# Kernel optimization log

Measured on AMD Instinct MI355X. Metric: run time of the kernel, lower is better.

## Reference

```python
import jax, jax.numpy as jnp
import numpy as np
from jax import lax

T, B, I, N, C, L = 512, 256, 64, 512, 10, 3
TAU = 2.0  # train_tau=False -> constant, non-trainable


def setup_inputs() -> dict:
    key = jax.random.key(0)
    ks = jax.random.split(key, 12)
    f32 = jnp.float32
    data = jax.random.normal(ks[0], (T, B, I), f32)
    h0 = 0.1 * jax.random.uniform(ks[1], (L, B, N), f32)  # matches 0.1*torch.rand init
    # Linear params; weights stored as [in, out] so y = x @ W + b
    Win = jax.random.normal(ks[2], (I, N), f32) / np.float32(np.sqrt(I))
    b_in = 0.01 * jax.random.normal(ks[3], (N,), f32)
    Whh = jax.random.normal(ks[4], (L, N, N), f32) / np.float32(np.sqrt(N))
    b_hh = 0.01 * jax.random.normal(ks[5], (L, N), f32)
    Whi = jax.random.normal(ks[6], (L - 1, N, N), f32) / np.float32(np.sqrt(N))
    b_hi = 0.01 * jax.random.normal(ks[7], (L - 1, N), f32)
    Wfc = jax.random.normal(ks[8], (N, C), f32) / np.float32(np.sqrt(N))
    b_fc = 0.01 * jax.random.normal(ks[9], (C,), f32)
    return {"data": data, "h0": h0, "Win": Win, "b_in": b_in,
            "Whh": Whh, "b_hh": b_hh, "Whi": Whi, "b_hi": b_hi,
            "Wfc": Wfc, "b_fc": b_fc}


def reference(data, h0, Win, b_in, Whh, b_hh, Whi, b_hi, Wfc, b_fc):
    alpha = 1.0 - 1.0 / TAU
    # forward() zeroes the recurrent diagonal every call
    Whh = Whh * (1.0 - jnp.eye(N, dtype=Whh.dtype))
    x = data @ Win + b_in  # [T, B, N] input projection (single input layer, mean over 1)

    def step(hs, inp):
        h0_, h1_, h2_ = hs
        # layer 0: leaky integration + LeakyReLU; same inp fed to every layer
        n0 = jax.nn.leaky_relu(alpha * h0_ + (h0_ @ Whh[0] + b_hh[0] + inp) / TAU)
        # layer 1 sees the *updated* layer-0 state (sequential within a timestep)
        n1 = jax.nn.leaky_relu(
            alpha * h1_ + (h1_ @ Whh[1] + b_hh[1] + n0 @ Whi[0] + b_hi[0] + inp) / TAU)
        n2 = jax.nn.leaky_relu(
            alpha * h2_ + (h2_ @ Whh[2] + b_hh[2] + n1 @ Whi[1] + b_hi[1] + inp) / TAU)
        return (n0, n1, n2), None

    hs_final, _ = lax.scan(step, (h0[0], h0[1], h0[2]), x)
    out = hs_final[-1] @ Wfc + b_fc  # [B, C], single readout head
    return out
```

## Files before the change

### kernel.cpp

```cpp
#include <hip/hip_runtime.h>
#include <stdint.h>


#define TS    512
#define BB    256
#define NN    512
#define MR    16
#define NRG   16
#define NCT   4
#define RD    8

#define SW(r, c) (((r) << 9) + ((((c) ^ ((r) & 7))) << 3))

typedef __attribute__((ext_vector_type(8))) short s8v;
typedef __attribute__((ext_vector_type(4))) float f4v;
typedef __attribute__((ext_vector_type(4))) unsigned int u4v;

#define MFMA16(a, b, c) __builtin_amdgcn_mfma_f32_16x16x32_bf16((a), (b), (c), 0, 0, 0)

__device__ __forceinline__ short f2bf(float f) {
  union { float f; unsigned u; } v; v.f = f;
  unsigned u = v.u;
  u += 0x7fffu + ((u >> 16) & 1u);
  return (short)(u >> 16);
}

__device__ __forceinline__ s8v pack8(f4v a, f4v b) {
  s8v v;
  v[0] = f2bf(a[0]); v[1] = f2bf(a[1]); v[2] = f2bf(a[2]); v[3] = f2bf(a[3]);
  v[4] = f2bf(b[0]); v[5] = f2bf(b[1]); v[6] = f2bf(b[2]); v[7] = f2bf(b[3]);
  return v;
}

__device__ __forceinline__ void waitvm0() {
  asm volatile("s_waitcnt vmcnt(0)" ::: "memory");
}

__device__ __forceinline__ void stg_sc1_b16(unsigned short* p, unsigned v) {
  asm volatile("global_store_short %0, %1, off sc1" :: "v"(p), "v"(v) : "memory");
}
__device__ __forceinline__ unsigned agent_ld(const unsigned* p) {
  return __hip_atomic_load(p, __ATOMIC_RELAXED, __HIP_MEMORY_SCOPE_AGENT);
}
__device__ __forceinline__ void agent_st(unsigned* p, unsigned v) {
  __hip_atomic_store(p, v, __ATOMIC_RELAXED, __HIP_MEMORY_SCOPE_AGENT);
}

__device__ __forceinline__ void ld4_dual(u4v o[4],
    unsigned vA, unsigned vB,
    const unsigned short* sq, const unsigned short* sp) {
  asm volatile(
      "global_load_dwordx4 %0, %4, %6 sc1\n\t"
      "global_load_dwordx4 %1, %5, %6 sc1\n\t"
      "global_load_dwordx4 %2, %4, %7 sc1\n\t"
      "global_load_dwordx4 %3, %5, %7 sc1\n\t"
      "s_waitcnt vmcnt(0)"
      : "=&v"(o[0]), "=&v"(o[1]), "=&v"(o[2]), "=&v"(o[3])
      : "v"(vA), "v"(vB), "s"(sq), "s"(sp)
      : "memory");
}
__device__ __forceinline__ void ld2_sync(u4v o[2],
    unsigned vA, unsigned vB, const unsigned short* sb) {
  asm volatile(
      "global_load_dwordx4 %0, %2, %4 sc1\n\t"
      "global_load_dwordx4 %1, %3, %4 sc1\n\t"
      "s_waitcnt vmcnt(0)"
      : "=&v"(o[0]), "=&v"(o[1])
      : "v"(vA), "v"(vB), "s"(sb)
      : "memory");
}

__global__ __launch_bounds__(512, 2) void rnn_pipe(
    const float* __restrict__ data, const float* __restrict__ h0,
    const float* __restrict__ Win,  const float* __restrict__ b_in,
    const float* __restrict__ Whh,  const float* __restrict__ b_hh,
    const float* __restrict__ Whi,  const float* __restrict__ b_hi,
    unsigned short* __restrict__ ring, unsigned* __restrict__ cnt,
    float* __restrict__ hfinal)
{
  __shared__ __attribute__((aligned(16))) unsigned short qtile[MR * NN];
  __shared__ __attribute__((aligned(16))) unsigned short ptile[MR * NN];

  const int bi   = blockIdx.x;
  const int x8   = bi & 7;
  const int rr   = bi >> 3;
  const int half = (rr >= 12) ? 1 : 0;
  const int m    = rr - half * 12;
  const int rg   = x8 * 2 + half;
  const int lay  = m >> 2;
  const int ct   = m & 3;
  const int tid  = threadIdx.x;
  const int wv   = tid >> 6;
  const int lane = tid & 63;
  const int lo   = lane & 15;
  const int q4   = lane >> 4;
  const int row0 = rg * MR;
  const int cw   = ct * 128 + wv * 16;

  const int sidx = (lay * NRG + rg) * NCT + ct;
  unsigned* selfprod = cnt + (size_t)sidx * 32;
  unsigned* selfdone = cnt + (size_t)(256 + sidx) * 32;

  unsigned* pollptr = selfprod;
  int polltype = 0;
  if (lane < 4) {
    pollptr = cnt + (size_t)((lay * NRG + rg) * NCT + lane) * 32;  polltype = 1;
  } else if (lane >= 4 && lane < 8 && lay > 0) {
    pollptr = cnt + (size_t)(((lay - 1) * NRG + rg) * NCT + (lane - 4)) * 32;  polltype = 2;
  } else if (lane >= 8 && lane < 12 && lay < 2) {
    pollptr = cnt + (size_t)(256 + ((lay + 1) * NRG + rg) * NCT + (lane - 8)) * 32;  polltype = 3;
  }

  s8v WH[16];
  s8v WI[16];
  s8v WX[2];
  float biasv;
  f4v  hst;

  {
    const float* WmH = Whh + (size_t)lay * NN * NN;
    const int col = cw + lo;
    #pragma unroll
    for (int kk = 0; kk < 16; ++kk) {
      s8v v;
      #pragma unroll
      for (int j = 0; j < 8; ++j) {
        const int k = kk * 32 + q4 * 8 + j;
        float f = WmH[(size_t)k * NN + col];
        if (k == col) f = 0.f;
        v[j] = f2bf(f);
      }
      WH[kk] = v;
    }
    if (lay > 0) {
      const float* WmI = Whi + (size_t)(lay - 1) * NN * NN;
      #pragma unroll
      for (int kk = 0; kk < 16; ++kk) {
        s8v v;
        #pragma unroll
        for (int j = 0; j < 8; ++j)
          v[j] = f2bf(WmI[(size_t)(kk * 32 + q4 * 8 + j) * NN + col]);
        WI[kk] = v;
      }
    }
    #pragma unroll
    for (int kk = 0; kk < 2; ++kk) {
      s8v v;
      #pragma unroll
      for (int j = 0; j < 8; ++j)
        v[j] = f2bf(Win[(size_t)(kk * 32 + q4 * 8 + j) * NN + col]);
      WX[kk] = v;
    }
    float b = b_hh[lay * NN + col] + b_in[col];
    if (lay > 0) b += b_hi[(lay - 1) * NN + col];
    biasv = b;
    #pragma unroll
    for (int r = 0; r < 4; ++r)
      hst[r] = h0[(size_t)lay * BB * NN + (size_t)(row0 + q4 * 4 + r) * NN + col];
  }

  const size_t myring = (size_t)(lay * NRG + rg) * RD;
  const size_t upring = (size_t)((lay - 1) * NRG + rg) * RD;

  unsigned voffA = (unsigned)((0 * 512 + tid) * 16);
  unsigned voffB = (unsigned)((1 * 512 + tid) * 16);
  const int gA_r = tid >> 6,           gA_c = tid & 63;
  const int gB_r = (512 + tid) >> 6,   gB_c = tid & 63;

  f4v xa0, xa1, xa2, xa3;
  {
    const float* dsrc = data + ((size_t)0 * BB + row0 + lo) * 64 + q4 * 8;
    xa0 = *(const f4v*)(dsrc + 0);
    xa1 = *(const f4v*)(dsrc + 4);
    xa2 = *(const f4v*)(dsrc + 32);
    xa3 = *(const f4v*)(dsrc + 36);
  }

  for (int t = 0; t < TS; ++t) {
    f4v zero4 = {0.f, 0.f, 0.f, 0.f};
    f4v accQ = zero4;
    f4v accP = zero4;
    {
      s8v xv0 = pack8(xa0, xa1);
      s8v xv1 = pack8(xa2, xa3);
      accQ = MFMA16(xv0, WX[0], accQ);
      accQ = MFMA16(xv1, WX[1], accQ);
    }

    unsigned tgt = 0;
    if (polltype == 1) tgt = (unsigned)t;
    else if (polltype == 2) tgt = (unsigned)(t + 1);
    else if (polltype == 3 && t >= RD) tgt = (unsigned)(t - RD + 1);
    for (;;) {
      unsigned v = agent_ld(pollptr);
      if (__all((int)(v >= tgt))) break;
    }

    {
      const unsigned short* qsrc = ring + (myring + ((t - 1) & (RD - 1))) * (MR * NN);
      const unsigned short* psrc = ring + (upring + (t & (RD - 1))) * (MR * NN);
      if (t >= 1 && lay > 0) {
        u4v st[4];
        ld4_dual(st, voffA, voffB, qsrc, psrc);
        *(u4v*)(qtile + SW(gA_r, gA_c)) = st[0];
        *(u4v*)(qtile + SW(gB_r, gB_c)) = st[1];
        *(u4v*)(ptile + SW(gA_r, gA_c)) = st[2];
        *(u4v*)(ptile + SW(gB_r, gB_c)) = st[3];
      } else if (t >= 1) {
        u4v st[2];
        ld2_sync(st, voffA, voffB, qsrc);
        *(u4v*)(qtile + SW(gA_r, gA_c)) = st[0];
        *(u4v*)(qtile + SW(gB_r, gB_c)) = st[1];
      } else if (lay > 0) {
        u4v st[2];
        ld2_sync(st, voffA, voffB, psrc);
        *(u4v*)(ptile + SW(gA_r, gA_c)) = st[0];
        *(u4v*)(ptile + SW(gB_r, gB_c)) = st[1];
      }
    }
    __syncthreads();
    if (tid == 0 && lay > 0)
      agent_st(selfdone, (unsigned)(t + 1));

    if (lay > 0) {
      #pragma unroll
      for (int kk = 0; kk < 16; ++kk) {
        s8v av = *(const s8v*)(ptile + SW(lo, kk * 4 + q4));
        accP = MFMA16(av, WI[kk], accP);
      }
    }
    if (t == 0) {
      const float* hsrc = h0 + (size_t)lay * BB * NN + (size_t)(row0 + lo) * NN + q4 * 8;
      #pragma unroll
      for (int kk = 0; kk < 16; ++kk) {
        f4v a = *(const f4v*)(hsrc + kk * 32);
        f4v b = *(const f4v*)(hsrc + kk * 32 + 4);
        s8v av = pack8(a, b);
        accQ = MFMA16(av, WH[kk], accQ);
      }
    } else {
      #pragma unroll
      for (int kk = 0; kk < 16; ++kk) {
        s8v av = *(const s8v*)(qtile + SW(lo, kk * 4 + q4));
        accQ = MFMA16(av, WH[kk], accQ);
      }
    }

    {
      unsigned short* rslot = ring + (myring + (t & (RD - 1))) * (MR * NN);
      const int col = cw + lo;
      #pragma unroll
      for (int r = 0; r < 4; ++r) {
        const int row = q4 * 4 + r;
        float v = 0.5f * hst[r] + 0.5f * (accQ[r] + accP[r] + biasv);
        v = (v >= 0.f) ? v : 0.01f * v;
        hst[r] = v;
        stg_sc1_b16(rslot + (size_t)row * NN + col,
                    (unsigned)(unsigned short)f2bf(v));
        if (lay == 2 && t == TS - 1)
          hfinal[(size_t)(row0 + row) * NN + col] = v;
      }
    }

    {
      const int tn = (t + 1 < TS) ? t + 1 : t;
      const float* dsrc = data + ((size_t)tn * BB + row0 + lo) * 64 + q4 * 8;
      xa0 = *(const f4v*)(dsrc + 0);
      xa1 = *(const f4v*)(dsrc + 4);
      xa2 = *(const f4v*)(dsrc + 32);
      xa3 = *(const f4v*)(dsrc + 36);
    }
    waitvm0();
    __syncthreads();
    if (tid == 0)
      agent_st(selfprod, (unsigned)(t + 1));
  }
}

__global__ void readout_k(const float* __restrict__ hfinal, const float* __restrict__ Wfc,
                          const float* __restrict__ b_fc, float* __restrict__ out)
{
  const int row = blockIdx.x;
  const int lane = threadIdx.x;
  float a[10];
  #pragma unroll
  for (int c = 0; c < 10; ++c) a[c] = 0.f;
  for (int k = lane; k < NN; k += 64) {
    const float h = hfinal[(size_t)row * NN + k];
    const float* w = Wfc + (size_t)k * 10;
    #pragma unroll
    for (int c = 0; c < 10; ++c) a[c] += h * w[c];
  }
  #pragma unroll
  for (int off = 32; off > 0; off >>= 1) {
    #pragma unroll
    for (int c = 0; c < 10; ++c) a[c] += __shfl_down(a[c], off);
  }
  if (lane == 0) {
    #pragma unroll
    for (int c = 0; c < 10; ++c) out[row * 10 + c] = a[c] + b_fc[c];
  }
}

extern "C" void kernel_launch(void* const* d_in, const int* in_sizes, int n_in,
                              void* d_out, int out_size, void* d_ws, size_t ws_size,
                              hipStream_t stream) {
  (void)in_sizes; (void)n_in; (void)out_size; (void)ws_size;
  const float* data = (const float*)d_in[0];
  const float* h0   = (const float*)d_in[1];
  const float* Win  = (const float*)d_in[2];
  const float* b_in = (const float*)d_in[3];
  const float* Whh  = (const float*)d_in[4];
  const float* b_hh = (const float*)d_in[5];
  const float* Whi  = (const float*)d_in[6];
  const float* b_hi = (const float*)d_in[7];
  const float* Wfc  = (const float*)d_in[8];
  const float* b_fc = (const float*)d_in[9];

  unsigned short* ring = (unsigned short*)d_ws;
  const size_t ring_bytes = (size_t)3 * NRG * RD * MR * NN * 2;
  unsigned* cnt = (unsigned*)((char*)d_ws + ring_bytes);
  float* hfinal = (float*)((char*)d_ws + ring_bytes + 65536);

  hipMemsetAsync(cnt, 0, 65536, stream);
  hipLaunchKernelGGL(rnn_pipe, dim3(192), dim3(512), 0, stream,
                     data, h0, Win, b_in, Whh, b_hh, Whi, b_hi, ring, cnt, hfinal);
  hipLaunchKernelGGL(readout_k, dim3(256), dim3(64), 0, stream,
                     hfinal, Wfc, b_fc, (float*)d_out);
}
```

Measured before the change: 1.980 ms.

## Split each layer's columns across two 1024-thread blocks instead of four

Each (layer, row-group) is now handled by 2 blocks of 1024 threads (96 blocks total) rather than 4 blocks of 512. Each block owns 256 output columns and writes them to its own ring slot, and the state tile is gathered from its own slot plus its sibling's. With half as many producers, fewer flag polls and cross-block exchanges are needed per step, which shortens the per-timestep synchronisation on the serial critical path. The cost is fewer blocks sharing the work, so each block does more per step and overall parallelism drops; register pressure at 1024 threads may also limit the weights held per wave.

```diff
diff --git a/kernel.cpp b/kernel.cpp
--- a/kernel.cpp
+++ b/kernel.cpp
@@ -7,8 +7,9 @@
 #define NN    512
 #define MR    16
 #define NRG   16
-#define NCT   4
+#define NHF   2
 #define RD    8
+#define SLOTS 4096
 
 #define SW(r, c) (((r) << 9) + ((((c) ^ ((r) & 7))) << 3))
 
@@ -46,31 +47,27 @@
   __hip_atomic_store(p, v, __ATOMIC_RELAXED, __HIP_MEMORY_SCOPE_AGENT);
 }
 
-__device__ __forceinline__ void ld4_dual(u4v o[4],
-    unsigned vA, unsigned vB,
-    const unsigned short* sq, const unsigned short* sp) {
-  asm volatile(
-      "global_load_dwordx4 %0, %4, %6 sc1\n\t"
-      "global_load_dwordx4 %1, %5, %6 sc1\n\t"
-      "global_load_dwordx4 %2, %4, %7 sc1\n\t"
-      "global_load_dwordx4 %3, %5, %7 sc1\n\t"
-      "s_waitcnt vmcnt(0)"
-      : "=&v"(o[0]), "=&v"(o[1]), "=&v"(o[2]), "=&v"(o[3])
-      : "v"(vA), "v"(vB), "s"(sq), "s"(sp)
-      : "memory");
-}
 __device__ __forceinline__ void ld2_sync(u4v o[2],
-    unsigned vA, unsigned vB, const unsigned short* sb) {
+    unsigned vq, unsigned vp, const unsigned short* ringbase) {
   asm volatile(
       "global_load_dwordx4 %0, %2, %4 sc1\n\t"
       "global_load_dwordx4 %1, %3, %4 sc1\n\t"
       "s_waitcnt vmcnt(0)"
       : "=&v"(o[0]), "=&v"(o[1])
-      : "v"(vA), "v"(vB), "s"(sb)
+      : "v"(vq), "v"(vp), "s"(ringbase)
       : "memory");
 }
-
-__global__ __launch_bounds__(512, 2) void rnn_pipe(
+__device__ __forceinline__ void ld1_sync(u4v o[1],
+    unsigned voff, const unsigned short* ringbase) {
+  asm volatile(
+      "global_load_dwordx4 %0, %1, %2 sc1\n\t"
+      "s_waitcnt vmcnt(0)"
+      : "=&v"(o[0])
+      : "v"(voff), "s"(ringbase)
+      : "memory");
+}
+
+__global__ __launch_bounds__(1024, 1) void rnn_pipe(
     const float* __restrict__ data, const float* __restrict__ h0,
     const float* __restrict__ Win,  const float* __restrict__ b_in,
     const float* __restrict__ Whh,  const float* __restrict__ b_hh,
@@ -83,32 +80,33 @@
 
   const int bi   = blockIdx.x;
   const int x8   = bi & 7;
-  const int rr   = bi >> 3;
-  const int half = (rr >= 12) ? 1 : 0;
-  const int m    = rr - half * 12;
-  const int rg   = x8 * 2 + half;
-  const int lay  = m >> 2;
-  const int ct   = m & 3;
+  const int rest = bi >> 3;
+  const int hrg  = (rest >= 6) ? 1 : 0;
+  const int m    = rest - hrg * 6;
+  const int rg   = x8 * 2 + hrg;
+  const int lay  = m >> 1;
+  const int hf   = m & 1;
   const int tid  = threadIdx.x;
   const int wv   = tid >> 6;
   const int lane = tid & 63;
   const int lo   = lane & 15;
   const int q4   = lane >> 4;
   const int row0 = rg * MR;
-  const int cw   = ct * 128 + wv * 16;
-
-  const int sidx = (lay * NRG + rg) * NCT + ct;
+  const int cl   = wv * 16 + lo;
+  const int col  = hf * 256 + cl;
+
+  const int sidx = (lay * NRG + rg) * NHF + hf;
   unsigned* selfprod = cnt + (size_t)sidx * 32;
   unsigned* selfdone = cnt + (size_t)(256 + sidx) * 32;
 
   unsigned* pollptr = selfprod;
   int polltype = 0;
-  if (lane < 4) {
-    pollptr = cnt + (size_t)((lay * NRG + rg) * NCT + lane) * 32;  polltype = 1;
-  } else if (lane >= 4 && lane < 8 && lay > 0) {
-    pollptr = cnt + (size_t)(((lay - 1) * NRG + rg) * NCT + (lane - 4)) * 32;  polltype = 2;
-  } else if (lane >= 8 && lane < 12 && lay < 2) {
-    pollptr = cnt + (size_t)(256 + ((lay + 1) * NRG + rg) * NCT + (lane - 8)) * 32;  polltype = 3;
+  if (lane == 0) {
+    pollptr = cnt + (size_t)((lay * NRG + rg) * NHF + (1 - hf)) * 32;          polltype = 1;
+  } else if (lane >= 4 && lane < 6 && lay > 0) {
+    pollptr = cnt + (size_t)(((lay - 1) * NRG + rg) * NHF + (lane - 4)) * 32;  polltype = 2;
+  } else if (lane >= 8 && lane < 10 && lay < 2) {
+    pollptr = cnt + (size_t)(256 + ((lay + 1) * NRG + rg) * NHF + (lane - 8)) * 32;  polltype = 3;
   }
 
   s8v WH[16];
@@ -119,7 +117,6 @@
 
   {
     const float* WmH = Whh + (size_t)lay * NN * NN;
-    const int col = cw + lo;
     #pragma unroll
     for (int kk = 0; kk < 16; ++kk) {
       s8v v;
@@ -159,13 +156,16 @@
       hst[r] = h0[(size_t)lay * BB * NN + (size_t)(row0 + q4 * 4 + r) * NN + col];
   }
 
-  const size_t myring = (size_t)(lay * NRG + rg) * RD;
-  const size_t upring = (size_t)((lay - 1) * NRG + rg) * RD;
-
-  unsigned voffA = (unsigned)((0 * 512 + tid) * 16);
-  unsigned voffB = (unsigned)((1 * 512 + tid) * 16);
-  const int gA_r = tid >> 6,           gA_c = tid & 63;
-  const int gB_r = (512 + tid) >> 6,   gB_c = tid & 63;
+  const int myring  = sidx * RD;
+  const int sibring = ((lay * NRG + rg) * NHF + (1 - hf)) * RD;
+  const int upring0 = (lay > 0) ? (((lay - 1) * NRG + rg) * NHF + 0) * RD : 0;
+  const int upring1 = (lay > 0) ? (((lay - 1) * NRG + rg) * NHF + 1) * RD : 0;
+
+  const int sg_r   = tid >> 6;
+  const int sg_c   = tid & 63;
+  const unsigned lstat = (unsigned)(sg_r * 512 + (sg_c & 31) * 16);
+  const int qmine  = ((sg_c >> 5) == hf);
+  const int puse1  = (sg_c >> 5);
 
   f4v xa0, xa1, xa2, xa3;
   {
@@ -197,25 +197,25 @@
     }
 
     {
-      const unsigned short* qsrc = ring + (myring + ((t - 1) & (RD - 1))) * (MR * NN);
-      const unsigned short* psrc = ring + (upring + (t & (RD - 1))) * (MR * NN);
+      const unsigned qslot_my  = (unsigned)((myring  + ((t - 1) & (RD - 1))) * (SLOTS * 2));
+      const unsigned qslot_sib = (unsigned)((sibring + ((t - 1) & (RD - 1))) * (SLOTS * 2));
+      const unsigned pslot_0   = (unsigned)((upring0 + (t & (RD - 1))) * (SLOTS * 2));
+      const unsigned pslot_1   = (unsigned)((upring1 + (t & (RD - 1))) * (SLOTS * 2));
+      const unsigned vq = (qmine ? qslot_my : qslot_sib) + lstat;
+      const unsigned vp = (puse1 ? pslot_1 : pslot_0) + lstat;
       if (t >= 1 && lay > 0) {
-        u4v st[4];
-        ld4_dual(st, voffA, voffB, qsrc, psrc);
-        *(u4v*)(qtile + SW(gA_r, gA_c)) = st[0];
-        *(u4v*)(qtile + SW(gB_r, gB_c)) = st[1];
-        *(u4v*)(ptile + SW(gA_r, gA_c)) = st[2];
-        *(u4v*)(ptile + SW(gB_r, gB_c)) = st[3];
+        u4v st[2];
+        ld2_sync(st, vq, vp, ring);
+        *(u4v*)(qtile + SW(sg_r, sg_c)) = st[0];
+        *(u4v*)(ptile + SW(sg_r, sg_c)) = st[1];
       } else if (t >= 1) {
-        u4v st[2];
-        ld2_sync(st, voffA, voffB, qsrc);
-        *(u4v*)(qtile + SW(gA_r, gA_c)) = st[0];
-        *(u4v*)(qtile + SW(gB_r, gB_c)) = st[1];
+        u4v st[1];
+        ld1_sync(st, vq, ring);
+        *(u4v*)(qtile + SW(sg_r, sg_c)) = st[0];
       } else if (lay > 0) {
-        u4v st[2];
-        ld2_sync(st, voffA, voffB, psrc);
-        *(u4v*)(ptile + SW(gA_r, gA_c)) = st[0];
-        *(u4v*)(ptile + SW(gB_r, gB_c)) = st[1];
+        u4v st[1];
+        ld1_sync(st, vp, ring);
+        *(u4v*)(ptile + SW(sg_r, sg_c)) = st[0];
       }
     }
     __syncthreads();
@@ -247,15 +247,14 @@
     }
 
     {
-      unsigned short* rslot = ring + (myring + (t & (RD - 1))) * (MR * NN);
-      const int col = cw + lo;
+      unsigned short* rslot = ring + (size_t)(myring + (t & (RD - 1))) * SLOTS;
       #pragma unroll
       for (int r = 0; r < 4; ++r) {
         const int row = q4 * 4 + r;
         float v = 0.5f * hst[r] + 0.5f * (accQ[r] + accP[r] + biasv);
         v = (v >= 0.f) ? v : 0.01f * v;
         hst[r] = v;
-        stg_sc1_b16(rslot + (size_t)row * NN + col,
+        stg_sc1_b16(rslot + (size_t)row * 256 + cl,
                     (unsigned)(unsigned short)f2bf(v));
         if (lay == 2 && t == TS - 1)
           hfinal[(size_t)(row0 + row) * NN + col] = v;
@@ -318,12 +317,12 @@
   const float* b_fc = (const float*)d_in[9];
 
   unsigned short* ring = (unsigned short*)d_ws;
-  const size_t ring_bytes = (size_t)3 * NRG * RD * MR * NN * 2;
+  const size_t ring_bytes = (size_t)3 * NRG * NHF * RD * SLOTS * 2;
   unsigned* cnt = (unsigned*)((char*)d_ws + ring_bytes);
   float* hfinal = (float*)((char*)d_ws + ring_bytes + 65536);
 
   hipMemsetAsync(cnt, 0, 65536, stream);
-  hipLaunchKernelGGL(rnn_pipe, dim3(192), dim3(512), 0, stream,
+  hipLaunchKernelGGL(rnn_pipe, dim3(96), dim3(1024), 0, stream,
                      data, h0, Win, b_in, Whh, b_hh, Whi, b_hi, ring, cnt, hfinal);
   hipLaunchKernelGGL(readout_k, dim3(256), dim3(64), 0, stream,
                      hfinal, Wfc, b_fc, (float*)d_out);
```

Measured after the change: 6.405 ms. 3.24x slower.
